# Optimization experiments

Measured on AMD Instinct MI355X. Metric: run time of the kernel, lower is better.

## Reference

```python
import jax, jax.numpy as jnp
import numpy as np

B, S, HID = 2, 4096, 3584
NH, NKV, HD, FD = 16, 8, 256, 64
CHUNK = 64

def _rope_tables(seq_len, dim, base=10000.0):
    inv = 1.0 / (base ** (np.arange(0, dim, 2) / dim))      # [dim/2]
    f = np.outer(np.arange(seq_len), inv)                   # [S, dim/2]
    return jnp.asarray(np.cos(f), jnp.float32), jnp.asarray(np.sin(f), jnp.float32)

def setup_inputs() -> dict:
    key = jax.random.key(0)
    ks = jax.random.split(key, 8)
    def w(k, shape, fan):
        return jax.random.normal(k, shape, jnp.float32) * (fan ** -0.5)
    cos, sin = _rope_tables(S, HD)
    return dict(
        hidden_states=jax.random.normal(ks[0], (B, S, HID), jnp.float32),
        cos=cos, sin=sin,
        Wq=w(ks[1], (HID, NH * HD), HID),
        Wk=w(ks[2], (HID, NKV * HD), HID),
        Wv=w(ks[3], (HID, NKV * HD), HID),
        Wo=w(ks[4], (NH * HD, HID), NH * HD),
        fmq=w(ks[5], (NH, HD, FD), HD),
        fmk=w(ks[6], (NH, HD, FD), HD),
    )

def apply_rope(x, cos, sin):
    # Gemma split-half rotary. x: [B,S,h,D]; cos/sin: [S,D/2]
    d2 = x.shape[-1] // 2
    x1, x2 = x[..., :d2], x[..., d2:]
    c = cos[None, :, None, :]
    s = sin[None, :, None, :]
    return jnp.concatenate([x1 * c - x2 * s, x1 * s + x2 * c], axis=-1)

def feature_map(x, w):
    # Hedgehog: per-head linear then cat(softmax(z), softmax(-z)).
    # x: [B,h,S,D], w: [h,D,F] -> [B,h,S,2F]
    z = jnp.einsum('bhsd,hdf->bhsf', x, w)
    return jnp.concatenate([jax.nn.softmax(z, axis=-1), jax.nn.softmax(-z, axis=-1)], axis=-1)

def chunk_linear_attn(q, k, v, chunk=CHUNK):
    # q,k: [B,H,T,dk]; v: [B,H,T,dv]; T divisible by chunk (S=4096, chunk=64)
    b, h, T, dk = q.shape
    dv = v.shape[-1]
    n = T // chunk
    q = q.reshape(b, h, n, chunk, dk) * (dk ** -0.5)
    k = k.reshape(b, h, n, chunk, dk)
    v = v.reshape(b, h, n, chunk, dv)
    kv = jnp.einsum('bhncd,bhnce->bhnde', k, v)          # per-chunk K^T V: [b,h,n,dk,dv]
    kv = jnp.cumsum(kv, axis=2)
    kv = jnp.concatenate([jnp.zeros_like(kv[:, :, :1]), kv[:, :, :-1]], axis=2)  # exclusive
    inter = jnp.einsum('bhncd,bhnde->bhnce', q, kv)
    scores = jnp.einsum('bhncd,bhnkd->bhnck', q, k)
    causal = jnp.tril(jnp.ones((chunk, chunk), dtype=bool))
    scores = jnp.where(causal, scores, jnp.zeros((), scores.dtype))
    intra = jnp.einsum('bhnck,bhnke->bhnce', scores, v)
    return (inter + intra).reshape(b, h, T, dv)

def reference(hidden_states, cos, sin, Wq, Wk, Wv, Wo, fmq, fmk):
    b, s, _ = hidden_states.shape
    q = (hidden_states @ Wq).reshape(b, s, NH, HD)
    k = (hidden_states @ Wk).reshape(b, s, NKV, HD)
    v = (hidden_states @ Wv).reshape(b, s, NKV, HD)
    q = apply_rope(q, cos, sin)
    k = apply_rope(k, cos, sin)
    g = NH // NKV
    k = jnp.repeat(k, g, axis=2)   # GQA expansion
    v = jnp.repeat(v, g, axis=2)
    q = q.transpose(0, 2, 1, 3)    # [B,H,S,D]
    k = k.transpose(0, 2, 1, 3)
    v = v.transpose(0, 2, 1, 3)
    q = feature_map(q, fmq)        # [B,H,S,2F]
    k = feature_map(k, fmk)
    o = chunk_linear_attn(q, k, v)                      # [B,H,S,HD]
    o = o.transpose(0, 2, 1, 3).reshape(b, s, NH * HD)
    return o @ Wo
```

## Files before the change

kernel.cpp:

```cpp
#include <hip/hip_runtime.h>

typedef float  f32x4  __attribute__((ext_vector_type(4)));
typedef __bf16 bf16x4 __attribute__((ext_vector_type(4)));
typedef __bf16 bf16x8 __attribute__((ext_vector_type(8)));

#define MFMA16(a,b,c) __builtin_amdgcn_mfma_f32_16x16x32_bf16((a),(b),(c),0,0,0)

__device__ __forceinline__ void async_copy16(void* lds, const void* gmem) {
  __builtin_amdgcn_global_load_lds(
      (const __attribute__((address_space(1))) void*)gmem,
      (__attribute__((address_space(3))) void*)lds, 16, 0, 0);
}

template<int N> __device__ __forceinline__ void vmcnt_gate() {
  if constexpr (N == 8) asm volatile("s_waitcnt vmcnt(8)" ::: "memory");
  else if constexpr (N == 6) asm volatile("s_waitcnt vmcnt(6)" ::: "memory");
  else if constexpr (N == 4) asm volatile("s_waitcnt vmcnt(4)" ::: "memory");
  else if constexpr (N == 2) asm volatile("s_waitcnt vmcnt(2)" ::: "memory");
  else if constexpr (N == 0) asm volatile("s_waitcnt vmcnt(0)" ::: "memory");
  __builtin_amdgcn_sched_barrier(0);
}

#define LGKM(N) do { __builtin_amdgcn_sched_barrier(0); \
                     asm volatile("s_waitcnt lgkmcnt(" #N ")" ::: "memory"); \
                     __builtin_amdgcn_sched_barrier(0); } while (0)

#define BARRIER do { __builtin_amdgcn_sched_barrier(0); \
                     __builtin_amdgcn_s_barrier(); \
                     __builtin_amdgcn_sched_barrier(0); } while (0)

__global__ __launch_bounds__(256) void convert_kernel(const float* __restrict__ in,
                                                      __bf16* __restrict__ out, size_t n4) {
  size_t i = (size_t)blockIdx.x * 256 + threadIdx.x;
  if (i >= n4) return;
  f32x4 v = *(const f32x4*)(in + i * 4);
  bf16x4 o;
  #pragma unroll
  for (int j = 0; j < 4; ++j) o[j] = (__bf16)v[j];
  *(bf16x4*)(out + i * 4) = o;
}

__global__ __launch_bounds__(256) void transpose_kernel(const float* __restrict__ in,
                                                        __bf16* __restrict__ out, int R, int C) {
  __shared__ float tile[32][33];
  int bx = blockIdx.x, by = blockIdx.y;
  int tx = threadIdx.x & 31, ty0 = threadIdx.x >> 5;
  #pragma unroll
  for (int i = 0; i < 4; ++i) {
    int r = by * 32 + ty0 + i * 8;
    tile[ty0 + i * 8][tx] = in[(size_t)r * C + bx * 32 + tx];
  }
  __syncthreads();
  #pragma unroll
  for (int i = 0; i < 4; ++i) {
    int c = bx * 32 + ty0 + i * 8;
    out[(size_t)c * R + by * 32 + tx] = (__bf16)tile[tx][ty0 + i * 8];
  }
}


__device__ __forceinline__ void stage_q(__bf16* region, int qrow, const __bf16* src,
                                        int K, int w, int l) {
  int r = qrow + w * 8 + (l >> 3);
  async_copy16(region + (size_t)(qrow + w * 8) * 64,
               src + (size_t)r * K + (((l & 7) ^ (r & 7)) << 3));
}

template<bool LATE, bool EARLY, bool NEXT, int G2, int G3>
__device__ __forceinline__ void tile_body(__bf16* smem,
                                          const __bf16* Apan, const __bf16* Bpan,
                                          int K, int tau, int wm, int wn,
                                          int lo, int hi, int w, int l,
                                          bf16x8 (&aA)[4], bf16x8 (&aB)[4],
                                          bf16x8 (&bA)[4], bf16x8 (&bB)[4],
                                          f32x4 (&acc)[8][4]) {
  const int buf = tau & 1, nbuf = buf ^ 1;
  __bf16* Ab = smem + buf * 32768;
  __bf16* Bb = Ab + 16384;
  __bf16* An = smem + nbuf * 32768;
  __bf16* Bn = An + 16384;

  #pragma unroll
  for (int t = 0; t < 4; ++t) {
    int ra = wm * 128 + 64 + t * 16 + lo;
    aB[t] = *(const bf16x8*)(Ab + (size_t)ra * 64 + ((hi ^ (ra & 7)) << 3));
  }
  if constexpr (LATE) {
    const __bf16* Ap1 = Apan + (size_t)(tau + 1) * 64;
    stage_q(An, 64,  Ap1, K, w, l);
    stage_q(An, 192, Ap1, K, w, l);
  }
  LGKM(4);
  __builtin_amdgcn_s_setprio(1);
  #pragma unroll
  for (int mt = 0; mt < 4; ++mt)
    #pragma unroll
    for (int nt = 0; nt < 4; ++nt)
      acc[mt][nt] = MFMA16(aA[mt], bA[nt], acc[mt][nt]);
  __builtin_amdgcn_s_setprio(0);
  BARRIER;

  #pragma unroll
  for (int t = 0; t < 4; ++t) {
    int ra = wm * 128 + t * 16 + lo;
    aA[t] = *(const bf16x8*)(Ab + (size_t)ra * 64 + (((4 + hi) ^ (ra & 7)) << 3));
  }
  #pragma unroll
  for (int t = 0; t < 4; ++t) {
    int rb = wn * 64 + t * 16 + lo;
    bB[t] = *(const bf16x8*)(Bb + (size_t)rb * 64 + (((4 + hi) ^ (rb & 7)) << 3));
  }
  LGKM(8);
  __builtin_amdgcn_s_setprio(1);
  #pragma unroll
  for (int mt = 0; mt < 4; ++mt)
    #pragma unroll
    for (int nt = 0; nt < 4; ++nt)
      acc[4 + mt][nt] = MFMA16(aB[mt], bA[nt], acc[4 + mt][nt]);
  __builtin_amdgcn_s_setprio(0);
  BARRIER;

  #pragma unroll
  for (int t = 0; t < 4; ++t) {
    int ra = wm * 128 + 64 + t * 16 + lo;
    aB[t] = *(const bf16x8*)(Ab + (size_t)ra * 64 + (((4 + hi) ^ (ra & 7)) << 3));
  }
  LGKM(4);
  __builtin_amdgcn_s_setprio(1);
  #pragma unroll
  for (int mt = 0; mt < 4; ++mt)
    #pragma unroll
    for (int nt = 0; nt < 4; ++nt)
      acc[mt][nt] = MFMA16(aA[mt], bB[nt], acc[mt][nt]);
  __builtin_amdgcn_s_setprio(0);
  if constexpr (G2 >= 0) vmcnt_gate<G2>();
  BARRIER;

  if constexpr (NEXT) {
    #pragma unroll
    for (int t = 0; t < 4; ++t) {
      int ra = wm * 128 + t * 16 + lo;
      aA[t] = *(const bf16x8*)(An + (size_t)ra * 64 + ((hi ^ (ra & 7)) << 3));
    }
    #pragma unroll
    for (int t = 0; t < 4; ++t) {
      int rb = wn * 64 + t * 16 + lo;
      bA[t] = *(const bf16x8*)(Bn + (size_t)rb * 64 + ((hi ^ (rb & 7)) << 3));
    }
  }
  if constexpr (EARLY) {
    const __bf16* Ap2 = Apan + (size_t)(tau + 2) * 64;
    const __bf16* Bp2 = Bpan + (size_t)(tau + 2) * 64;
    stage_q(Ab, 0,   Ap2, K, w, l);
    stage_q(Ab, 128, Ap2, K, w, l);
    stage_q(Bb, 0,   Bp2, K, w, l);
    stage_q(Bb, 64,  Bp2, K, w, l);
    stage_q(Bb, 128, Bp2, K, w, l);
    stage_q(Bb, 192, Bp2, K, w, l);
  }
  if constexpr (NEXT) LGKM(8); else LGKM(0);
  __builtin_amdgcn_s_setprio(1);
  #pragma unroll
  for (int mt = 0; mt < 4; ++mt)
    #pragma unroll
    for (int nt = 0; nt < 4; ++nt)
      acc[4 + mt][nt] = MFMA16(aB[mt], bB[nt], acc[4 + mt][nt]);
  __builtin_amdgcn_s_setprio(0);
  if constexpr (G3 >= 0) vmcnt_gate<G3>();
  BARRIER;
}

template <typename CT>
__global__ __launch_bounds__(512, 2) void gemm256_kernel(const __bf16* __restrict__ A,
                                                         const __bf16* __restrict__ Bt,
                                                         CT* __restrict__ C, int M, int N, int K) {
  extern __shared__ __bf16 smem[];

  const int gx = gridDim.x;
  const int nwg = gx * gridDim.y;
  const int wg = blockIdx.y * gx + blockIdx.x;
  const int qq = nwg >> 3;
  const int id2 = (wg & 7) * qq + (wg >> 3);
  const int m0 = (id2 / gx) * 256, n0 = (id2 % gx) * 256;

  const int tid = threadIdx.x;
  const int l = tid & 63, w = tid >> 6;
  const int lo = l & 15, hi = l >> 4;
  const int wm = w >> 2, wn = w & 3;

  const __bf16* Apan = A + (size_t)m0 * K;
  const __bf16* Bpan = Bt + (size_t)n0 * K;

  f32x4 acc[8][4] = {};
  bf16x8 aA[4], aB[4], bA[4], bB[4];

  stage_q(smem,          0,   Apan, K, w, l);
  stage_q(smem,          128, Apan, K, w, l);
  stage_q(smem + 16384,  0,   Bpan, K, w, l);
  stage_q(smem + 16384,  64,  Bpan, K, w, l);
  stage_q(smem + 16384,  128, Bpan, K, w, l);
  stage_q(smem + 16384,  192, Bpan, K, w, l);
  stage_q(smem,          64,  Apan, K, w, l);
  stage_q(smem,          192, Apan, K, w, l);
  stage_q(smem + 32768,  0,   Apan + 64, K, w, l);
  stage_q(smem + 32768,  128, Apan + 64, K, w, l);
  stage_q(smem + 49152,  0,   Bpan + 64, K, w, l);
  stage_q(smem + 49152,  64,  Bpan + 64, K, w, l);
  stage_q(smem + 49152,  128, Bpan + 64, K, w, l);
  stage_q(smem + 49152,  192, Bpan + 64, K, w, l);
  stage_q(smem + 32768,  64,  Apan + 64, K, w, l);
  stage_q(smem + 32768,  192, Apan + 64, K, w, l);
  vmcnt_gate<8>();
  BARRIER;

  #pragma unroll
  for (int t = 0; t < 4; ++t) {
    int ra = wm * 128 + t * 16 + lo;
    aA[t] = *(const bf16x8*)(smem + (size_t)ra * 64 + ((hi ^ (ra & 7)) << 3));
  }
  #pragma unroll
  for (int t = 0; t < 4; ++t) {
    int rb = wn * 64 + t * 16 + lo;
    bA[t] = *(const bf16x8*)(smem + 16384 + (size_t)rb * 64 + ((hi ^ (rb & 7)) << 3));
  }

  const int T = K >> 6;
  tile_body<false, true,  true,  2,  6>(smem, Apan, Bpan, K, 0,     wm, wn, lo, hi, w, l, aA, aB, bA, bB, acc);
  for (int tau = 1; tau < T - 2; ++tau)
    tile_body<true, true,  true,  2,  6>(smem, Apan, Bpan, K, tau,   wm, wn, lo, hi, w, l, aA, aB, bA, bB, acc);
  tile_body<true,  false, true,  2,  0>(smem, Apan, Bpan, K, T - 2, wm, wn, lo, hi, w, l, aA, aB, bA, bB, acc);
  tile_body<false, false, false, -1, -1>(smem, Apan, Bpan, K, T - 1, wm, wn, lo, hi, w, l, aA, aB, bA, bB, acc);

  #pragma unroll
  for (int mt = 0; mt < 8; ++mt)
    #pragma unroll
    for (int nt = 0; nt < 4; ++nt) {
      int col = n0 + wn * 64 + nt * 16 + lo;
      #pragma unroll
      for (int r = 0; r < 4; ++r) {
        int row = m0 + wm * 128 + mt * 16 + 4 * hi + r;
        C[(size_t)row * N + col] = (CT)acc[mt][nt][r];
      }
    }
}

__global__ __launch_bounds__(256) void rope_kernel(const __bf16* __restrict__ qin,
                                                   const float* __restrict__ cosT,
                                                   const float* __restrict__ sinT,
                                                   __bf16* __restrict__ outp, int H, int bshift) {
  int idx = blockIdx.x * 256 + threadIdx.x;
  int j = idx & 31;
  int s = (idx >> 5) & 4095;
  int h = (idx >> 17) & (H - 1);
  int b = idx >> bshift;
  int d = j * 4;
  size_t ibase = ((size_t)(b * 4096 + s)) * (H * 256) + h * 256 + d;
  bf16x4 x1 = *(const bf16x4*)&qin[ibase];
  bf16x4 x2 = *(const bf16x4*)&qin[ibase + 128];
  f32x4 c  = *(const f32x4*)&cosT[s * 128 + d];
  f32x4 sn = *(const f32x4*)&sinT[s * 128 + d];
  bf16x4 o1, o2;
  #pragma unroll
  for (int t = 0; t < 4; ++t) {
    float a = (float)x1[t], bb = (float)x2[t];
    o1[t] = (__bf16)(a * c[t] - bb * sn[t]);
    o2[t] = (__bf16)(a * sn[t] + bb * c[t]);
  }
  size_t obase = (((size_t)(b * H + h)) * 4096 + s) * 256 + d;
  *(bf16x4*)&outp[obase] = o1;
  *(bf16x4*)&outp[obase + 128] = o2;
}

__global__ __launch_bounds__(256) void vperm_kernel(const __bf16* __restrict__ in,
                                                    __bf16* __restrict__ out) {
  int idx = blockIdx.x * 256 + threadIdx.x;
  int j = idx & 31;
  int s = (idx >> 5) & 4095;
  int kv = (idx >> 17) & 7;
  int b = idx >> 20;
  bf16x8 v = *(const bf16x8*)&in[((size_t)(b * 4096 + s)) * 2048 + kv * 256 + j * 8];
  *(bf16x8*)&out[(((size_t)(b * 8 + kv)) * 4096 + s) * 256 + j * 8] = v;
}

__global__ __launch_bounds__(256) void fm_kernel(const __bf16* __restrict__ rope,
                                                 const float* __restrict__ fm,
                                                 __bf16* __restrict__ out, int srcH, float scale) {
  __shared__ __bf16 fmT[64][256];
  int bh = blockIdx.y;
  int h = bh & 15, b = bh >> 4;
  int s0 = blockIdx.x * 128;
  int tid = threadIdx.x, lane = tid & 63, wid = tid >> 6, hi = lane >> 4, lo = lane & 15;

  const float* fmh = fm + (size_t)h * 256 * 64;
  for (int i = tid; i < 256 * 64; i += 256) {
    int d = i >> 6, f = i & 63;
    fmT[f][(((d >> 3) ^ (f & 7)) << 3) | (d & 7)] = (__bf16)fmh[i];
  }
  __syncthreads();

  int srch = (srcH == 16) ? h : (h >> 1);
  const __bf16* abase = rope + ((size_t)(b * srcH + srch) * 4096 + s0 + 32 * wid) * 256;
  f32x4 acc[2][4] = {};
  for (int kk = 0; kk < 256; kk += 32) {
    bf16x8 a[2], bf[4];
    #pragma unroll
    for (int mt = 0; mt < 2; ++mt)
      a[mt] = *(const bf16x8*)(abase + (size_t)(16 * mt + lo) * 256 + kk + 8 * hi);
    const int G = (kk >> 3) + hi;
    #pragma unroll
    for (int nt = 0; nt < 4; ++nt) {
      int f = 16 * nt + lo;
      bf[nt] = *(const bf16x8*)&fmT[f][(G ^ (f & 7)) << 3];
    }
    #pragma unroll
    for (int mt = 0; mt < 2; ++mt)
      #pragma unroll
      for (int nt = 0; nt < 4; ++nt)
        acc[mt][nt] = MFMA16(a[mt], bf[nt], acc[mt][nt]);
  }

  size_t obase = ((size_t)(b * 16 + h) * 4096 + s0 + 32 * wid);
  #pragma unroll
  for (int mt = 0; mt < 2; ++mt) {
    #pragma unroll
    for (int r = 0; r < 4; ++r) {
      float z0 = acc[mt][0][r], z1 = acc[mt][1][r], z2 = acc[mt][2][r], z3 = acc[mt][3][r];
      float mx = fmaxf(fmaxf(z0, z1), fmaxf(z2, z3));
      float mn = fminf(fminf(z0, z1), fminf(z2, z3));
      #pragma unroll
      for (int off = 1; off < 16; off <<= 1) {
        mx = fmaxf(mx, __shfl_xor(mx, off));
        mn = fminf(mn, __shfl_xor(mn, off));
      }
      float ep0 = __expf(z0 - mx), ep1 = __expf(z1 - mx), ep2 = __expf(z2 - mx), ep3 = __expf(z3 - mx);
      float en0 = __expf(mn - z0), en1 = __expf(mn - z1), en2 = __expf(mn - z2), en3 = __expf(mn - z3);
      float sp = ep0 + ep1 + ep2 + ep3, sn = en0 + en1 + en2 + en3;
      #pragma unroll
      for (int off = 1; off < 16; off <<= 1) {
        sp += __shfl_xor(sp, off);
        sn += __shfl_xor(sn, off);
      }
      float rp = scale / sp, rn = scale / sn;
      int row = 16 * mt + 4 * hi + r;
      __bf16* op = out + (obase + row) * 128;
      op[0  + lo] = (__bf16)(ep0 * rp);  op[16 + lo] = (__bf16)(ep1 * rp);
      op[32 + lo] = (__bf16)(ep2 * rp);  op[48 + lo] = (__bf16)(ep3 * rp);
      op[64 + lo] = (__bf16)(en0 * rn);  op[80 + lo] = (__bf16)(en1 * rn);
      op[96 + lo] = (__bf16)(en2 * rn);  op[112 + lo] = (__bf16)(en3 * rn);
    }
  }
}

__global__ __launch_bounds__(256) void attn_kernel(const __bf16* __restrict__ qf,
                                                   const __bf16* __restrict__ kf,
                                                   const __bf16* __restrict__ vp,
                                                   __bf16* __restrict__ o) {
  __shared__ __bf16 k_s[64][128];
  __shared__ __bf16 vT_s[32][64];
  __shared__ __bf16 sc_s[64][64];
  __shared__ __bf16 STb[32][128];

  int bid = blockIdx.x;
  int dvb = bid & 7, h = (bid >> 3) & 15, b = bid >> 7;
  int dv0 = dvb * 32;
  int tid = threadIdx.x, lane = tid & 63, wid = tid >> 6, hi = lane >> 4, lo = lane & 15;

  const __bf16* qh = qf + ((size_t)(b * 16 + h)) * 4096 * 128;
  const __bf16* kh = kf + ((size_t)(b * 16 + h)) * 4096 * 128;
  const __bf16* vh = vp + ((size_t)(b * 8 + (h >> 1))) * 4096 * 256 + dv0;
  __bf16* oh = o + ((size_t)b * 4096) * 4096 + h * 256 + dv0;

  {
    unsigned int* z = (unsigned int*)&STb[0][0];
    for (int i = tid; i < 2048; i += 256) z[i] = 0u;
  }
  f32x4 st[2][2] = {};

  for (int n = 0; n < 64; ++n) {
    int s0 = n * 64;
    #pragma unroll
    for (int i = 0; i < 4; ++i) {
      int rb = (wid * 4 + i) * 4;
      int r = rb + (lane >> 4);
      int Glog = (lane & 15) ^ (r & 7);
      async_copy16(&k_s[rb][0], kh + (size_t)(s0 + r) * 128 + Glog * 8);
    }
    {
      int c = tid >> 2, d8 = (tid & 3) * 8;
      bf16x8 vv = *(const bf16x8*)(vh + (size_t)(s0 + c) * 256 + d8);
      #pragma unroll
      for (int j = 0; j < 8; ++j) {
        int dv = d8 + j;
        vT_s[dv][(((c >> 3) ^ (dv & 7)) << 3) | (c & 7)] = vv[j];
      }
    }
    __syncthreads();

    bf16x8 aq[4];
    #pragma unroll
    for (int kq = 0; kq < 4; ++kq)
      aq[kq] = *(const bf16x8*)(qh + (size_t)(s0 + 16 * wid + lo) * 128 + 32 * kq + 8 * hi);

    f32x4 acc_o[2] = {}, sacc[4] = {};
    #pragma unroll
    for (int nt = 0; nt < 2; ++nt)
      #pragma unroll
      for (int kq = 0; kq < 4; ++kq) {
        int rr = 16 * nt + lo, G = 4 * kq + hi;
        bf16x8 bf = *(const bf16x8*)&STb[rr][(G ^ (rr & 7)) << 3];
        acc_o[nt] = MFMA16(aq[kq], bf, acc_o[nt]);
      }
    #pragma unroll
    for (int nt = 0; nt < 4; ++nt)
      #pragma unroll
      for (int kq = 0; kq < 4; ++kq) {
        int rr = 16 * nt + lo, G = 4 * kq + hi;
        bf16x8 bf = *(const bf16x8*)&k_s[rr][(G ^ (rr & 7)) << 3];
        sacc[nt] = MFMA16(aq[kq], bf, sacc[nt]);
      }
    #pragma unroll
    for (int nt = 0; nt < 4; ++nt)
      #pragma unroll
      for (int r = 0; r < 4; ++r) {
        int c = 16 * wid + 4 * hi + r;
        int cp = 16 * nt + lo;
        float v = (cp <= c) ? sacc[nt][r] : 0.0f;
        sc_s[c][(((cp >> 3) ^ (c & 7)) << 3) | (cp & 7)] = (__bf16)v;
      }
    asm volatile("" ::: "memory");
    #pragma unroll
    for (int nt = 0; nt < 2; ++nt)
      #pragma unroll
      for (int kq = 0; kq < 2; ++kq) {
        int rA = 16 * wid + lo, GA = 4 * kq + hi;
        bf16x8 af = *(const bf16x8*)&sc_s[rA][(GA ^ (rA & 7)) << 3];
        int rB = 16 * nt + lo;
        bf16x8 bf = *(const bf16x8*)&vT_s[rB][(GA ^ (rB & 7)) << 3];
        acc_o[nt] = MFMA16(af, bf, acc_o[nt]);
      }
    #pragma unroll
    for (int nt = 0; nt < 2; ++nt)
      #pragma unroll
      for (int r = 0; r < 4; ++r) {
        int c = 16 * wid + 4 * hi + r;
        oh[(size_t)(s0 + c) * 4096 + 16 * nt + lo] = (__bf16)acc_o[nt][r];
      }
    __syncthreads();

    bf16x8 bu[2][2];
    #pragma unroll
    for (int q = 0; q < 2; ++q) {
      int dk = 16 * (2 * wid + q) + lo;
      #pragma unroll
      for (int kq = 0; kq < 2; ++kq) {
        bf16x8 tmp;
        #pragma unroll
        for (int j = 0; j < 8; ++j) {
          int c = 32 * kq + 8 * hi + j;
          tmp[j] = k_s[c][(((dk >> 3) ^ (c & 7)) << 3) | (dk & 7)];
        }
        bu[q][kq] = tmp;
      }
    }
    #pragma unroll
    for (int mt = 0; mt < 2; ++mt)
      #pragma unroll
      for (int kq = 0; kq < 2; ++kq) {
        int rA = 16 * mt + lo, GA = 4 * kq + hi;
        bf16x8 av = *(const bf16x8*)&vT_s[rA][(GA ^ (rA & 7)) << 3];
        #pragma unroll
        for (int q = 0; q < 2; ++q)
          st[mt][q] = MFMA16(av, bu[q][kq], st[mt][q]);
      }
    #pragma unroll
    for (int mt = 0; mt < 2; ++mt)
      #pragma unroll
      for (int q = 0; q < 2; ++q) {
        int dk = 16 * (2 * wid + q) + lo;
        #pragma unroll
        for (int r = 0; r < 4; ++r) {
          int dvr = 16 * mt + 4 * hi + r;
          STb[dvr][(((dk >> 3) ^ (dvr & 7)) << 3) | (dk & 7)] = (__bf16)st[mt][q][r];
        }
      }
    __syncthreads();
  }
}

extern "C" void kernel_launch(void* const* d_in, const int* in_sizes, int n_in,
                              void* d_out, int out_size, void* d_ws, size_t ws_size,
                              hipStream_t stream) {
  (void)in_sizes; (void)n_in; (void)out_size; (void)ws_size;
  const float* hs   = (const float*)d_in[0];
  const float* cosT = (const float*)d_in[1];
  const float* sinT = (const float*)d_in[2];
  const float* Wq   = (const float*)d_in[3];
  const float* Wk   = (const float*)d_in[4];
  const float* Wv   = (const float*)d_in[5];
  const float* Wo   = (const float*)d_in[6];
  const float* fmq  = (const float*)d_in[7];
  const float* fmk  = (const float*)d_in[8];
  float* out = (float*)d_out;
  char* ws = (char*)d_ws;

  hipFuncSetAttribute((const void*)gemm256_kernel<__bf16>,
                      hipFuncAttributeMaxDynamicSharedMemorySize, 131072);
  hipFuncSetAttribute((const void*)gemm256_kernel<float>,
                      hipFuncAttributeMaxDynamicSharedMemorySize, 131072);

  const size_t MB = 1024ull * 1024ull;
  __bf16* Xb   = (__bf16*)(ws + 0);
  __bf16* ropq = (__bf16*)(ws + 0);
  __bf16* Wqt  = (__bf16*)(ws + 70 * MB);
  __bf16* ropk = (__bf16*)(ws + 70 * MB);
  __bf16* Wkt  = (__bf16*)(ws + 104 * MB);
  __bf16* vpb  = (__bf16*)(ws + 104 * MB);
  __bf16* Wvt  = (__bf16*)(ws + 119 * MB);
  __bf16* Wot  = (__bf16*)(ws + 140 * MB);
  __bf16* Qb   = (__bf16*)(ws + 170 * MB);
  __bf16* ob   = (__bf16*)(ws + 170 * MB);
  __bf16* Kb   = (__bf16*)(ws + 238 * MB);
  __bf16* qfb  = (__bf16*)(ws + 238 * MB);
  __bf16* Vb   = (__bf16*)(ws + 272 * MB);
  __bf16* kfb  = (__bf16*)(ws + 272 * MB);

  convert_kernel<<<28672, 256, 0, stream>>>(hs, Xb, (size_t)8192 * 3584 / 4);
  transpose_kernel<<<dim3(128, 112), 256, 0, stream>>>(Wq, Wqt, 3584, 4096);
  transpose_kernel<<<dim3(64, 112),  256, 0, stream>>>(Wk, Wkt, 3584, 2048);
  transpose_kernel<<<dim3(64, 112),  256, 0, stream>>>(Wv, Wvt, 3584, 2048);
  transpose_kernel<<<dim3(112, 128), 256, 0, stream>>>(Wo, Wot, 4096, 3584);

  gemm256_kernel<__bf16><<<dim3(16, 32), 512, 131072, stream>>>(Xb, Wqt, Qb, 8192, 4096, 3584);
  gemm256_kernel<__bf16><<<dim3(8, 32),  512, 131072, stream>>>(Xb, Wkt, Kb, 8192, 2048, 3584);
  gemm256_kernel<__bf16><<<dim3(8, 32),  512, 131072, stream>>>(Xb, Wvt, Vb, 8192, 2048, 3584);

  rope_kernel<<<16384, 256, 0, stream>>>(Qb, cosT, sinT, ropq, 16, 21);
  rope_kernel<<<8192, 256, 0, stream>>>(Kb, cosT, sinT, ropk, 8, 20);
  vperm_kernel<<<8192, 256, 0, stream>>>(Vb, vpb);

  fm_kernel<<<dim3(32, 32), 256, 0, stream>>>(ropq, fmq, qfb, 16, 0.08838834764831845f);
  fm_kernel<<<dim3(32, 32), 256, 0, stream>>>(ropk, fmk, kfb, 8, 1.0f);

  attn_kernel<<<256, 256, 0, stream>>>(qfb, kfb, vpb, ob);

  gemm256_kernel<float><<<dim3(14, 32), 512, 131072, stream>>>(ob, Wot, out, 8192, 3584, 4096);
}
```

Before: 980.1 us.

## Simplify GEMM main loop to single register set with full lgkm waits

Reworks the 256x256 GEMM tile body to use one set of A/B fragment registers instead of double-buffered aA/aB/bA/bB. Fragment loads for the next MFMA block are no longer issued ahead of the current MFMAs. Every sub-step now waits for lgkmcnt(0) behind an extra barrier, and the vmcnt gating and prologue staging order are changed. This cuts register pressure and simplifies the code, but it removes the overlap of LDS reads with MFMA work and adds barriers.

```diff
diff --git a/kernel.cpp b/kernel.cpp
--- a/kernel.cpp
+++ b/kernel.cpp
@@ -15,19 +15,16 @@
 template<int N> __device__ __forceinline__ void vmcnt_gate() {
   if constexpr (N == 8) asm volatile("s_waitcnt vmcnt(8)" ::: "memory");
   else if constexpr (N == 6) asm volatile("s_waitcnt vmcnt(6)" ::: "memory");
-  else if constexpr (N == 4) asm volatile("s_waitcnt vmcnt(4)" ::: "memory");
   else if constexpr (N == 2) asm volatile("s_waitcnt vmcnt(2)" ::: "memory");
   else if constexpr (N == 0) asm volatile("s_waitcnt vmcnt(0)" ::: "memory");
   __builtin_amdgcn_sched_barrier(0);
 }
 
-#define LGKM(N) do { __builtin_amdgcn_sched_barrier(0); \
-                     asm volatile("s_waitcnt lgkmcnt(" #N ")" ::: "memory"); \
-                     __builtin_amdgcn_sched_barrier(0); } while (0)
+#define LGKM0 do { asm volatile("s_waitcnt lgkmcnt(0)" ::: "memory"); \
+                   __builtin_amdgcn_sched_barrier(0); } while (0)
 
 #define BARRIER do { __builtin_amdgcn_sched_barrier(0); \
-                     __builtin_amdgcn_s_barrier(); \
-                     __builtin_amdgcn_sched_barrier(0); } while (0)
+                     __builtin_amdgcn_s_barrier(); } while (0)
 
 __global__ __launch_bounds__(256) void convert_kernel(const float* __restrict__ in,
                                                       __bf16* __restrict__ out, size_t n4) {
@@ -66,87 +63,86 @@
                src + (size_t)r * K + (((l & 7) ^ (r & 7)) << 3));
 }
 
-template<bool LATE, bool EARLY, bool NEXT, int G2, int G3>
+template<bool LATE, bool EARLY, int G0, int G3>
 __device__ __forceinline__ void tile_body(__bf16* smem,
                                           const __bf16* Apan, const __bf16* Bpan,
                                           int K, int tau, int wm, int wn,
                                           int lo, int hi, int w, int l,
-                                          bf16x8 (&aA)[4], bf16x8 (&aB)[4],
-                                          bf16x8 (&bA)[4], bf16x8 (&bB)[4],
+                                          bf16x8 (&a)[4], bf16x8 (&b)[4],
                                           f32x4 (&acc)[8][4]) {
-  const int buf = tau & 1, nbuf = buf ^ 1;
+  const int buf = tau & 1;
   __bf16* Ab = smem + buf * 32768;
   __bf16* Bb = Ab + 16384;
-  __bf16* An = smem + nbuf * 32768;
-  __bf16* Bn = An + 16384;
-
-  #pragma unroll
-  for (int t = 0; t < 4; ++t) {
-    int ra = wm * 128 + 64 + t * 16 + lo;
-    aB[t] = *(const bf16x8*)(Ab + (size_t)ra * 64 + ((hi ^ (ra & 7)) << 3));
+  __bf16* An = smem + (buf ^ 1) * 32768;
+
+  #pragma unroll
+  for (int t = 0; t < 4; ++t) {
+    int ra = wm * 128 + t * 16 + lo;
+    a[t] = *(const bf16x8*)(Ab + (size_t)ra * 64 + ((hi ^ (ra & 7)) << 3));
+  }
+  #pragma unroll
+  for (int t = 0; t < 4; ++t) {
+    int rb = wn * 64 + t * 16 + lo;
+    b[t] = *(const bf16x8*)(Bb + (size_t)rb * 64 + ((hi ^ (rb & 7)) << 3));
   }
   if constexpr (LATE) {
     const __bf16* Ap1 = Apan + (size_t)(tau + 1) * 64;
     stage_q(An, 64,  Ap1, K, w, l);
     stage_q(An, 192, Ap1, K, w, l);
   }
-  LGKM(4);
+  BARRIER;
+  LGKM0;
   __builtin_amdgcn_s_setprio(1);
   #pragma unroll
   for (int mt = 0; mt < 4; ++mt)
     #pragma unroll
     for (int nt = 0; nt < 4; ++nt)
-      acc[mt][nt] = MFMA16(aA[mt], bA[nt], acc[mt][nt]);
+      acc[mt][nt] = MFMA16(a[mt], b[nt], acc[mt][nt]);
   __builtin_amdgcn_s_setprio(0);
+  if constexpr (G0 >= 0) vmcnt_gate<G0>();
+  BARRIER;
+
+  #pragma unroll
+  for (int t = 0; t < 4; ++t) {
+    int ra = wm * 128 + 64 + t * 16 + lo;
+    a[t] = *(const bf16x8*)(Ab + (size_t)ra * 64 + ((hi ^ (ra & 7)) << 3));
+  }
+  BARRIER;
+  LGKM0;
+  __builtin_amdgcn_s_setprio(1);
+  #pragma unroll
+  for (int mt = 0; mt < 4; ++mt)
+    #pragma unroll
+    for (int nt = 0; nt < 4; ++nt)
+      acc[4 + mt][nt] = MFMA16(a[mt], b[nt], acc[4 + mt][nt]);
+  __builtin_amdgcn_s_setprio(0);
   BARRIER;
 
   #pragma unroll
   for (int t = 0; t < 4; ++t) {
     int ra = wm * 128 + t * 16 + lo;
-    aA[t] = *(const bf16x8*)(Ab + (size_t)ra * 64 + (((4 + hi) ^ (ra & 7)) << 3));
+    a[t] = *(const bf16x8*)(Ab + (size_t)ra * 64 + (((4 + hi) ^ (ra & 7)) << 3));
   }
   #pragma unroll
   for (int t = 0; t < 4; ++t) {
     int rb = wn * 64 + t * 16 + lo;
-    bB[t] = *(const bf16x8*)(Bb + (size_t)rb * 64 + (((4 + hi) ^ (rb & 7)) << 3));
-  }
-  LGKM(8);
+    b[t] = *(const bf16x8*)(Bb + (size_t)rb * 64 + (((4 + hi) ^ (rb & 7)) << 3));
+  }
+  BARRIER;
+  LGKM0;
   __builtin_amdgcn_s_setprio(1);
   #pragma unroll
   for (int mt = 0; mt < 4; ++mt)
     #pragma unroll
     for (int nt = 0; nt < 4; ++nt)
-      acc[4 + mt][nt] = MFMA16(aB[mt], bA[nt], acc[4 + mt][nt]);
+      acc[mt][nt] = MFMA16(a[mt], b[nt], acc[mt][nt]);
   __builtin_amdgcn_s_setprio(0);
   BARRIER;
 
   #pragma unroll
   for (int t = 0; t < 4; ++t) {
     int ra = wm * 128 + 64 + t * 16 + lo;
-    aB[t] = *(const bf16x8*)(Ab + (size_t)ra * 64 + (((4 + hi) ^ (ra & 7)) << 3));
-  }
-  LGKM(4);
-  __builtin_amdgcn_s_setprio(1);
-  #pragma unroll
-  for (int mt = 0; mt < 4; ++mt)
-    #pragma unroll
-    for (int nt = 0; nt < 4; ++nt)
-      acc[mt][nt] = MFMA16(aA[mt], bB[nt], acc[mt][nt]);
-  __builtin_amdgcn_s_setprio(0);
-  if constexpr (G2 >= 0) vmcnt_gate<G2>();
-  BARRIER;
-
-  if constexpr (NEXT) {
-    #pragma unroll
-    for (int t = 0; t < 4; ++t) {
-      int ra = wm * 128 + t * 16 + lo;
-      aA[t] = *(const bf16x8*)(An + (size_t)ra * 64 + ((hi ^ (ra & 7)) << 3));
-    }
-    #pragma unroll
-    for (int t = 0; t < 4; ++t) {
-      int rb = wn * 64 + t * 16 + lo;
-      bA[t] = *(const bf16x8*)(Bn + (size_t)rb * 64 + ((hi ^ (rb & 7)) << 3));
-    }
+    a[t] = *(const bf16x8*)(Ab + (size_t)ra * 64 + (((4 + hi) ^ (ra & 7)) << 3));
   }
   if constexpr (EARLY) {
     const __bf16* Ap2 = Apan + (size_t)(tau + 2) * 64;
@@ -158,13 +154,14 @@
     stage_q(Bb, 128, Bp2, K, w, l);
     stage_q(Bb, 192, Bp2, K, w, l);
   }
-  if constexpr (NEXT) LGKM(8); else LGKM(0);
+  BARRIER;
+  LGKM0;
   __builtin_amdgcn_s_setprio(1);
   #pragma unroll
   for (int mt = 0; mt < 4; ++mt)
     #pragma unroll
     for (int nt = 0; nt < 4; ++nt)
-      acc[4 + mt][nt] = MFMA16(aB[mt], bB[nt], acc[4 + mt][nt]);
+      acc[4 + mt][nt] = MFMA16(a[mt], b[nt], acc[4 + mt][nt]);
   __builtin_amdgcn_s_setprio(0);
   if constexpr (G3 >= 0) vmcnt_gate<G3>();
   BARRIER;
@@ -192,44 +189,30 @@
   const __bf16* Bpan = Bt + (size_t)n0 * K;
 
   f32x4 acc[8][4] = {};
-  bf16x8 aA[4], aB[4], bA[4], bB[4];
+  bf16x8 a[4], b[4];
 
   stage_q(smem,          0,   Apan, K, w, l);
+  stage_q(smem,          64,  Apan, K, w, l);
   stage_q(smem,          128, Apan, K, w, l);
+  stage_q(smem,          192, Apan, K, w, l);
   stage_q(smem + 16384,  0,   Bpan, K, w, l);
   stage_q(smem + 16384,  64,  Bpan, K, w, l);
   stage_q(smem + 16384,  128, Bpan, K, w, l);
   stage_q(smem + 16384,  192, Bpan, K, w, l);
-  stage_q(smem,          64,  Apan, K, w, l);
-  stage_q(smem,          192, Apan, K, w, l);
   stage_q(smem + 32768,  0,   Apan + 64, K, w, l);
   stage_q(smem + 32768,  128, Apan + 64, K, w, l);
   stage_q(smem + 49152,  0,   Bpan + 64, K, w, l);
   stage_q(smem + 49152,  64,  Bpan + 64, K, w, l);
   stage_q(smem + 49152,  128, Bpan + 64, K, w, l);
   stage_q(smem + 49152,  192, Bpan + 64, K, w, l);
-  stage_q(smem + 32768,  64,  Apan + 64, K, w, l);
-  stage_q(smem + 32768,  192, Apan + 64, K, w, l);
-  vmcnt_gate<8>();
-  BARRIER;
-
-  #pragma unroll
-  for (int t = 0; t < 4; ++t) {
-    int ra = wm * 128 + t * 16 + lo;
-    aA[t] = *(const bf16x8*)(smem + (size_t)ra * 64 + ((hi ^ (ra & 7)) << 3));
-  }
-  #pragma unroll
-  for (int t = 0; t < 4; ++t) {
-    int rb = wn * 64 + t * 16 + lo;
-    bA[t] = *(const bf16x8*)(smem + 16384 + (size_t)rb * 64 + ((hi ^ (rb & 7)) << 3));
-  }
+  vmcnt_gate<6>();
+  BARRIER;
 
   const int T = K >> 6;
-  tile_body<false, true,  true,  2,  6>(smem, Apan, Bpan, K, 0,     wm, wn, lo, hi, w, l, aA, aB, bA, bB, acc);
-  for (int tau = 1; tau < T - 2; ++tau)
-    tile_body<true, true,  true,  2,  6>(smem, Apan, Bpan, K, tau,   wm, wn, lo, hi, w, l, aA, aB, bA, bB, acc);
-  tile_body<true,  false, true,  2,  0>(smem, Apan, Bpan, K, T - 2, wm, wn, lo, hi, w, l, aA, aB, bA, bB, acc);
-  tile_body<false, false, false, -1, -1>(smem, Apan, Bpan, K, T - 1, wm, wn, lo, hi, w, l, aA, aB, bA, bB, acc);
+  for (int tau = 0; tau < T - 2; ++tau)
+    tile_body<true,  true,  8, 8>(smem, Apan, Bpan, K, tau,   wm, wn, lo, hi, w, l, a, b, acc);
+  tile_body<true,  false, 8, 2>(smem, Apan, Bpan, K, T - 2, wm, wn, lo, hi, w, l, a, b, acc);
+  tile_body<false, false, 0, -1>(smem, Apan, Bpan, K, T - 1, wm, wn, lo, hi, w, l, a, b, acc);
 
   #pragma unroll
   for (int mt = 0; mt < 8; ++mt)
```

New measurement: 1.021 ms. 1.04x slower.

## Fuse RoPE and head-major permute into Q/K/V GEMM epilogues

Applied to the files above, without the earlier changes.

The Q and K projection GEMMs now apply split-half RoPE in their epilogue. To make that possible, the B-row loading is remapped so that each warp holds paired d and d+128 columns. The V GEMM writes directly in head-major layout. This removes the separate rope and vperm kernels and their round-trips of the Q/K/V intermediates through memory. In exchange, the epilogue does scattered per-element stores and cos/sin loads, and the workspace buffers are reassigned.

```diff
diff --git a/kernel.cpp b/kernel.cpp
--- a/kernel.cpp
+++ b/kernel.cpp
@@ -59,14 +59,16 @@
 }
 
 
+template<bool REMAP>
 __device__ __forceinline__ void stage_q(__bf16* region, int qrow, const __bf16* src,
                                         int K, int w, int l) {
-  int r = qrow + w * 8 + (l >> 3);
+  int s = qrow + w * 8 + (l >> 3);
+  int gr = REMAP ? (((s >> 5) << 4) | (s & 15) | (((s >> 4) & 1) << 7)) : s;
   async_copy16(region + (size_t)(qrow + w * 8) * 64,
-               src + (size_t)r * K + (((l & 7) ^ (r & 7)) << 3));
-}
-
-template<bool LATE, bool EARLY, bool NEXT, int G2, int G3>
+               src + (size_t)gr * K + (((l & 7) ^ (s & 7)) << 3));
+}
+
+template<bool LATE, bool EARLY, bool NEXT, int G2, int G3, bool BMAP>
 __device__ __forceinline__ void tile_body(__bf16* smem,
                                           const __bf16* Apan, const __bf16* Bpan,
                                           int K, int tau, int wm, int wn,
@@ -74,10 +76,10 @@
                                           bf16x8 (&aA)[4], bf16x8 (&aB)[4],
                                           bf16x8 (&bA)[4], bf16x8 (&bB)[4],
                                           f32x4 (&acc)[8][4]) {
-  const int buf = tau & 1, nbuf = buf ^ 1;
+  const int buf = tau & 1;
   __bf16* Ab = smem + buf * 32768;
   __bf16* Bb = Ab + 16384;
-  __bf16* An = smem + nbuf * 32768;
+  __bf16* An = smem + (buf ^ 1) * 32768;
   __bf16* Bn = An + 16384;
 
   #pragma unroll
@@ -87,8 +89,8 @@
   }
   if constexpr (LATE) {
     const __bf16* Ap1 = Apan + (size_t)(tau + 1) * 64;
-    stage_q(An, 64,  Ap1, K, w, l);
-    stage_q(An, 192, Ap1, K, w, l);
+    stage_q<false>(An, 64,  Ap1, K, w, l);
+    stage_q<false>(An, 192, Ap1, K, w, l);
   }
   LGKM(4);
   __builtin_amdgcn_s_setprio(1);
@@ -151,12 +153,12 @@
   if constexpr (EARLY) {
     const __bf16* Ap2 = Apan + (size_t)(tau + 2) * 64;
     const __bf16* Bp2 = Bpan + (size_t)(tau + 2) * 64;
-    stage_q(Ab, 0,   Ap2, K, w, l);
-    stage_q(Ab, 128, Ap2, K, w, l);
-    stage_q(Bb, 0,   Bp2, K, w, l);
-    stage_q(Bb, 64,  Bp2, K, w, l);
-    stage_q(Bb, 128, Bp2, K, w, l);
-    stage_q(Bb, 192, Bp2, K, w, l);
+    stage_q<false>(Ab, 0,   Ap2, K, w, l);
+    stage_q<false>(Ab, 128, Ap2, K, w, l);
+    stage_q<BMAP>(Bb, 0,   Bp2, K, w, l);
+    stage_q<BMAP>(Bb, 64,  Bp2, K, w, l);
+    stage_q<BMAP>(Bb, 128, Bp2, K, w, l);
+    stage_q<BMAP>(Bb, 192, Bp2, K, w, l);
   }
   if constexpr (NEXT) LGKM(8); else LGKM(0);
   __builtin_amdgcn_s_setprio(1);
@@ -170,11 +172,15 @@
   BARRIER;
 }
 
-template <typename CT>
+template <typename CT, int MODE>
 __global__ __launch_bounds__(512, 2) void gemm256_kernel(const __bf16* __restrict__ A,
                                                          const __bf16* __restrict__ Bt,
-                                                         CT* __restrict__ C, int M, int N, int K) {
+                                                         CT* __restrict__ C, int M, int N, int K,
+                                                         const float* __restrict__ cosT,
+                                                         const float* __restrict__ sinT,
+                                                         int Hh) {
   extern __shared__ __bf16 smem[];
+  constexpr bool BMAP = (MODE == 1);
 
   const int gx = gridDim.x;
   const int nwg = gx * gridDim.y;
@@ -194,22 +200,22 @@
   f32x4 acc[8][4] = {};
   bf16x8 aA[4], aB[4], bA[4], bB[4];
 
-  stage_q(smem,          0,   Apan, K, w, l);
-  stage_q(smem,          128, Apan, K, w, l);
-  stage_q(smem + 16384,  0,   Bpan, K, w, l);
-  stage_q(smem + 16384,  64,  Bpan, K, w, l);
-  stage_q(smem + 16384,  128, Bpan, K, w, l);
-  stage_q(smem + 16384,  192, Bpan, K, w, l);
-  stage_q(smem,          64,  Apan, K, w, l);
-  stage_q(smem,          192, Apan, K, w, l);
-  stage_q(smem + 32768,  0,   Apan + 64, K, w, l);
-  stage_q(smem + 32768,  128, Apan + 64, K, w, l);
-  stage_q(smem + 49152,  0,   Bpan + 64, K, w, l);
-  stage_q(smem + 49152,  64,  Bpan + 64, K, w, l);
-  stage_q(smem + 49152,  128, Bpan + 64, K, w, l);
-  stage_q(smem + 49152,  192, Bpan + 64, K, w, l);
-  stage_q(smem + 32768,  64,  Apan + 64, K, w, l);
-  stage_q(smem + 32768,  192, Apan + 64, K, w, l);
+  stage_q<false>(smem,          0,   Apan, K, w, l);
+  stage_q<false>(smem,          128, Apan, K, w, l);
+  stage_q<BMAP>(smem + 16384,  0,   Bpan, K, w, l);
+  stage_q<BMAP>(smem + 16384,  64,  Bpan, K, w, l);
+  stage_q<BMAP>(smem + 16384,  128, Bpan, K, w, l);
+  stage_q<BMAP>(smem + 16384,  192, Bpan, K, w, l);
+  stage_q<false>(smem,          64,  Apan, K, w, l);
+  stage_q<false>(smem,          192, Apan, K, w, l);
+  stage_q<false>(smem + 32768,  0,   Apan + 64, K, w, l);
+  stage_q<false>(smem + 32768,  128, Apan + 64, K, w, l);
+  stage_q<BMAP>(smem + 49152,  0,   Bpan + 64, K, w, l);
+  stage_q<BMAP>(smem + 49152,  64,  Bpan + 64, K, w, l);
+  stage_q<BMAP>(smem + 49152,  128, Bpan + 64, K, w, l);
+  stage_q<BMAP>(smem + 49152,  192, Bpan + 64, K, w, l);
+  stage_q<false>(smem + 32768,  64,  Apan + 64, K, w, l);
+  stage_q<false>(smem + 32768,  192, Apan + 64, K, w, l);
   vmcnt_gate<8>();
   BARRIER;
 
@@ -225,61 +231,58 @@
   }
 
   const int T = K >> 6;
-  tile_body<false, true,  true,  2,  6>(smem, Apan, Bpan, K, 0,     wm, wn, lo, hi, w, l, aA, aB, bA, bB, acc);
+  tile_body<false, true,  true,  2,  6, BMAP>(smem, Apan, Bpan, K, 0,     wm, wn, lo, hi, w, l, aA, aB, bA, bB, acc);
   for (int tau = 1; tau < T - 2; ++tau)
-    tile_body<true, true,  true,  2,  6>(smem, Apan, Bpan, K, tau,   wm, wn, lo, hi, w, l, aA, aB, bA, bB, acc);
-  tile_body<true,  false, true,  2,  0>(smem, Apan, Bpan, K, T - 2, wm, wn, lo, hi, w, l, aA, aB, bA, bB, acc);
-  tile_body<false, false, false, -1, -1>(smem, Apan, Bpan, K, T - 1, wm, wn, lo, hi, w, l, aA, aB, bA, bB, acc);
-
-  #pragma unroll
-  for (int mt = 0; mt < 8; ++mt)
-    #pragma unroll
-    for (int nt = 0; nt < 4; ++nt) {
-      int col = n0 + wn * 64 + nt * 16 + lo;
-      #pragma unroll
-      for (int r = 0; r < 4; ++r) {
-        int row = m0 + wm * 128 + mt * 16 + 4 * hi + r;
-        C[(size_t)row * N + col] = (CT)acc[mt][nt][r];
-      }
-    }
-}
-
-__global__ __launch_bounds__(256) void rope_kernel(const __bf16* __restrict__ qin,
-                                                   const float* __restrict__ cosT,
-                                                   const float* __restrict__ sinT,
-                                                   __bf16* __restrict__ outp, int H, int bshift) {
-  int idx = blockIdx.x * 256 + threadIdx.x;
-  int j = idx & 31;
-  int s = (idx >> 5) & 4095;
-  int h = (idx >> 17) & (H - 1);
-  int b = idx >> bshift;
-  int d = j * 4;
-  size_t ibase = ((size_t)(b * 4096 + s)) * (H * 256) + h * 256 + d;
-  bf16x4 x1 = *(const bf16x4*)&qin[ibase];
-  bf16x4 x2 = *(const bf16x4*)&qin[ibase + 128];
-  f32x4 c  = *(const f32x4*)&cosT[s * 128 + d];
-  f32x4 sn = *(const f32x4*)&sinT[s * 128 + d];
-  bf16x4 o1, o2;
-  #pragma unroll
-  for (int t = 0; t < 4; ++t) {
-    float a = (float)x1[t], bb = (float)x2[t];
-    o1[t] = (__bf16)(a * c[t] - bb * sn[t]);
-    o2[t] = (__bf16)(a * sn[t] + bb * c[t]);
-  }
-  size_t obase = (((size_t)(b * H + h)) * 4096 + s) * 256 + d;
-  *(bf16x4*)&outp[obase] = o1;
-  *(bf16x4*)&outp[obase + 128] = o2;
-}
-
-__global__ __launch_bounds__(256) void vperm_kernel(const __bf16* __restrict__ in,
-                                                    __bf16* __restrict__ out) {
-  int idx = blockIdx.x * 256 + threadIdx.x;
-  int j = idx & 31;
-  int s = (idx >> 5) & 4095;
-  int kv = (idx >> 17) & 7;
-  int b = idx >> 20;
-  bf16x8 v = *(const bf16x8*)&in[((size_t)(b * 4096 + s)) * 2048 + kv * 256 + j * 8];
-  *(bf16x8*)&out[(((size_t)(b * 8 + kv)) * 4096 + s) * 256 + j * 8] = v;
+    tile_body<true, true,  true,  2,  6, BMAP>(smem, Apan, Bpan, K, tau,   wm, wn, lo, hi, w, l, aA, aB, bA, bB, acc);
+  tile_body<true,  false, true,  2,  0, BMAP>(smem, Apan, Bpan, K, T - 2, wm, wn, lo, hi, w, l, aA, aB, bA, bB, acc);
+  tile_body<false, false, false, -1, -1, BMAP>(smem, Apan, Bpan, K, T - 1, wm, wn, lo, hi, w, l, aA, aB, bA, bB, acc);
+
+  if constexpr (MODE == 0) {
+    #pragma unroll
+    for (int mt = 0; mt < 8; ++mt)
+      #pragma unroll
+      for (int nt = 0; nt < 4; ++nt) {
+        int col = n0 + wn * 64 + nt * 16 + lo;
+        #pragma unroll
+        for (int r = 0; r < 4; ++r) {
+          int row = m0 + wm * 128 + mt * 16 + 4 * hi + r;
+          C[(size_t)row * N + col] = (CT)acc[mt][nt][r];
+        }
+      }
+  } else if constexpr (MODE == 2) {
+    const int kv = n0 >> 8;
+    #pragma unroll
+    for (int mt = 0; mt < 8; ++mt)
+      #pragma unroll
+      for (int nt = 0; nt < 4; ++nt) {
+        int col = wn * 64 + nt * 16 + lo;
+        #pragma unroll
+        for (int r = 0; r < 4; ++r) {
+          int row = m0 + wm * 128 + mt * 16 + 4 * hi + r;
+          int bb = row >> 12, sdx = row & 4095;
+          C[(((size_t)(bb * Hh + kv)) * 4096 + sdx) * 256 + col] = (CT)acc[mt][nt][r];
+        }
+      }
+  } else {
+    const int hq = n0 >> 8;
+    #pragma unroll
+    for (int mt = 0; mt < 8; ++mt)
+      #pragma unroll
+      for (int ntp = 0; ntp < 4; ntp += 2) {
+        int d = (2 * wn + (ntp >> 1)) * 16 + lo;
+        #pragma unroll
+        for (int r = 0; r < 4; ++r) {
+          int row = m0 + wm * 128 + mt * 16 + 4 * hi + r;
+          int bb = row >> 12, sdx = row & 4095;
+          float cc = cosT[(size_t)sdx * 128 + d];
+          float ss = sinT[(size_t)sdx * 128 + d];
+          float x1 = acc[mt][ntp][r], x2 = acc[mt][ntp + 1][r];
+          size_t base = (((size_t)(bb * Hh + hq)) * 4096 + sdx) * 256;
+          C[base + d]       = (CT)(x1 * cc - x2 * ss);
+          C[base + d + 128] = (CT)(x1 * ss + x2 * cc);
+        }
+      }
+  }
 }
 
 __global__ __launch_bounds__(256) void fm_kernel(const __bf16* __restrict__ rope,
@@ -503,26 +506,25 @@
   float* out = (float*)d_out;
   char* ws = (char*)d_ws;
 
-  hipFuncSetAttribute((const void*)gemm256_kernel<__bf16>,
+  hipFuncSetAttribute((const void*)gemm256_kernel<float, 0>,
                       hipFuncAttributeMaxDynamicSharedMemorySize, 131072);
-  hipFuncSetAttribute((const void*)gemm256_kernel<float>,
+  hipFuncSetAttribute((const void*)gemm256_kernel<__bf16, 1>,
+                      hipFuncAttributeMaxDynamicSharedMemorySize, 131072);
+  hipFuncSetAttribute((const void*)gemm256_kernel<__bf16, 2>,
                       hipFuncAttributeMaxDynamicSharedMemorySize, 131072);
 
   const size_t MB = 1024ull * 1024ull;
   __bf16* Xb   = (__bf16*)(ws + 0);
-  __bf16* ropq = (__bf16*)(ws + 0);
+  __bf16* qfb  = (__bf16*)(ws + 0);
+  __bf16* kfb  = (__bf16*)(ws + 34 * MB);
   __bf16* Wqt  = (__bf16*)(ws + 70 * MB);
-  __bf16* ropk = (__bf16*)(ws + 70 * MB);
+  __bf16* ob   = (__bf16*)(ws + 70 * MB);
   __bf16* Wkt  = (__bf16*)(ws + 104 * MB);
-  __bf16* vpb  = (__bf16*)(ws + 104 * MB);
   __bf16* Wvt  = (__bf16*)(ws + 119 * MB);
   __bf16* Wot  = (__bf16*)(ws + 140 * MB);
-  __bf16* Qb   = (__bf16*)(ws + 170 * MB);
-  __bf16* ob   = (__bf16*)(ws + 170 * MB);
-  __bf16* Kb   = (__bf16*)(ws + 238 * MB);
-  __bf16* qfb  = (__bf16*)(ws + 238 * MB);
-  __bf16* Vb   = (__bf16*)(ws + 272 * MB);
-  __bf16* kfb  = (__bf16*)(ws + 272 * MB);
+  __bf16* ropq = (__bf16*)(ws + 170 * MB);
+  __bf16* ropk = (__bf16*)(ws + 238 * MB);
+  __bf16* vpb  = (__bf16*)(ws + 272 * MB);
 
   convert_kernel<<<28672, 256, 0, stream>>>(hs, Xb, (size_t)8192 * 3584 / 4);
   transpose_kernel<<<dim3(128, 112), 256, 0, stream>>>(Wq, Wqt, 3584, 4096);
@@ -530,18 +532,18 @@
   transpose_kernel<<<dim3(64, 112),  256, 0, stream>>>(Wv, Wvt, 3584, 2048);
   transpose_kernel<<<dim3(112, 128), 256, 0, stream>>>(Wo, Wot, 4096, 3584);
 
-  gemm256_kernel<__bf16><<<dim3(16, 32), 512, 131072, stream>>>(Xb, Wqt, Qb, 8192, 4096, 3584);
-  gemm256_kernel<__bf16><<<dim3(8, 32),  512, 131072, stream>>>(Xb, Wkt, Kb, 8192, 2048, 3584);
-  gemm256_kernel<__bf16><<<dim3(8, 32),  512, 131072, stream>>>(Xb, Wvt, Vb, 8192, 2048, 3584);
-
-  rope_kernel<<<16384, 256, 0, stream>>>(Qb, cosT, sinT, ropq, 16, 21);
-  rope_kernel<<<8192, 256, 0, stream>>>(Kb, cosT, sinT, ropk, 8, 20);
-  vperm_kernel<<<8192, 256, 0, stream>>>(Vb, vpb);
+  gemm256_kernel<__bf16, 1><<<dim3(16, 32), 512, 131072, stream>>>(
+      Xb, Wqt, ropq, 8192, 4096, 3584, cosT, sinT, 16);
+  gemm256_kernel<__bf16, 1><<<dim3(8, 32),  512, 131072, stream>>>(
+      Xb, Wkt, ropk, 8192, 2048, 3584, cosT, sinT, 8);
+  gemm256_kernel<__bf16, 2><<<dim3(8, 32),  512, 131072, stream>>>(
+      Xb, Wvt, vpb, 8192, 2048, 3584, nullptr, nullptr, 8);
 
   fm_kernel<<<dim3(32, 32), 256, 0, stream>>>(ropq, fmq, qfb, 16, 0.08838834764831845f);
   fm_kernel<<<dim3(32, 32), 256, 0, stream>>>(ropk, fmk, kfb, 8, 1.0f);
 
   attn_kernel<<<256, 256, 0, stream>>>(qfb, kfb, vpb, ob);
 
-  gemm256_kernel<float><<<dim3(14, 32), 512, 131072, stream>>>(ob, Wot, out, 8192, 3584, 4096);
-}
+  gemm256_kernel<float, 0><<<dim3(14, 32), 512, 131072, stream>>>(
+      ob, Wot, out, 8192, 3584, 4096, nullptr, nullptr, 0);
+}
```

Measured after the change: 957.7 us. -2.3%, faster.
